# Kernel optimization log

Measured on AMD Instinct MI355X. Metric: run time of the kernel, lower is better.

Reference implementation:

```python
import jax, jax.numpy as jnp
from jax import lax
import numpy as np

NUM_ITER = 10
SMOOTH = 1.0
BCE_W, DICE_W, CLDICE_W = 0.3, 0.3, 0.4


def _maxpool(x, wh, ww):
    # x: (B, 1, H, W); 'SAME' padding with -inf identity == F.max_pool2d with zero-like pad of padding=(wh//2, ww//2)
    return lax.reduce_window(x, -jnp.inf, lax.max,
                             (1, 1, wh, ww), (1, 1, 1, 1), 'SAME')


def soft_erode(x):
    # min over vertical 3x1 and horizontal 1x3 windows, then elementwise min
    p1 = -_maxpool(-x, 3, 1)
    p2 = -_maxpool(-x, 1, 3)
    return jnp.minimum(p1, p2)


def soft_dilate(x):
    return _maxpool(x, 3, 3)


def soft_open(x):
    return soft_dilate(soft_erode(x))


def soft_skeleton(x):
    skel = jax.nn.relu(x - soft_open(x))
    er = x
    for _ in range(NUM_ITER):  # fixed, small trip count -> unrolled
        er = soft_erode(er)
        delta = jax.nn.relu(er - soft_open(er))
        skel = skel + jax.nn.relu(delta - skel * delta)
    return skel


def setup_inputs() -> dict:
    key = jax.random.key(0)
    k1, k2 = jax.random.split(key)
    B, H, W = 16, 1024, 1024
    pred = jax.random.normal(k1, (B, 1, H, W), dtype=jnp.float32)
    target = (jax.random.uniform(k2, (B, 1, H, W)) < 0.3).astype(jnp.float32)
    return {"pred": pred, "target": target}


def reference(pred, target):
    p = jax.nn.sigmoid(pred)
    y = target
    # BCEWithLogitsLoss (mean reduction, no pos_weight)
    bce = -jnp.mean(y * jax.nn.log_sigmoid(pred) + (1.0 - y) * jax.nn.log_sigmoid(-pred))
    # soft Dice over flattened tensors
    inter = jnp.sum(p * y)
    dice = (2.0 * inter + SMOOTH) / (jnp.sum(p) + jnp.sum(y) + SMOOTH)
    dice_loss = 1.0 - dice
    # clDice via soft skeletonization of both maps
    skel_pred = soft_skeleton(p)
    skel_tgt = soft_skeleton(y)
    tprec = (jnp.sum(skel_pred * y) + SMOOTH) / (jnp.sum(skel_pred) + SMOOTH)
    tsens = (jnp.sum(skel_tgt * p) + SMOOTH) / (jnp.sum(skel_tgt) + SMOOTH)
    cl_dice = 2.0 * tprec * tsens / (tprec + tsens + 1e-07)
    cldice_loss = 1.0 - cl_dice
    return BCE_W * bce + DICE_W * dice_loss + CLDICE_W * cldice_loss
```

## Files before the change

### kernel.cpp

```cpp
#include <hip/hip_runtime.h>
#include <hip/hip_fp16.h>
#include <math.h>

#define H_IMG 1024
#define W_IMG 1024
#define N_B   16
#define NPIX  (H_IMG * W_IMG)
#define N_TOT (16LL * NPIX)

#define TILE 64
#define HALO 12
#define RG   88
#define HST  92
#define SLOTS 32

#define PK_NINF 0xFC00FC00u
#define PK_SGN  0x80008000u

__device__ __forceinline__ float sigm(float x)  { return 1.0f / (1.0f + __expf(-x)); }

__device__ __forceinline__ unsigned pk_min(unsigned a, unsigned b) {
    unsigned r; asm("v_pk_min_f16 %0, %1, %2" : "=v"(r) : "v"(a), "v"(b)); return r;
}
__device__ __forceinline__ unsigned pk_max(unsigned a, unsigned b) {
    unsigned r; asm("v_pk_max_f16 %0, %1, %2" : "=v"(r) : "v"(a), "v"(b)); return r;
}
__device__ __forceinline__ unsigned pk_add(unsigned a, unsigned b) {
    unsigned r; asm("v_pk_add_f16 %0, %1, %2" : "=v"(r) : "v"(a), "v"(b)); return r;
}
__device__ __forceinline__ unsigned pk_fma(unsigned a, unsigned b, unsigned c) {
    unsigned r; asm("v_pk_fma_f16 %0, %1, %2, %3" : "=v"(r) : "v"(a), "v"(b), "v"(c)); return r;
}
__device__ __forceinline__ unsigned alignb(unsigned hi, unsigned lo) {
    unsigned r; asm("v_alignbit_b32 %0, %1, %2, 16" : "=v"(r) : "v"(hi), "v"(lo)); return r;
}

union H2U { __half2 h; unsigned u; };

__device__ __forceinline__ uint2 ld2u(const __half* p) { return *(const uint2*)p; }
__device__ __forceinline__ void  st2u(__half* p, unsigned a, unsigned b) { *(uint2*)p = make_uint2(a, b); }
__device__ __forceinline__ void st4h(__half* p, float x, float y, float z, float w) {
    H2U a, b;
    a.h = __floats2half2_rn(x, y);
    b.h = __floats2half2_rn(z, w);
    *(uint2*)p = make_uint2(a.u, b.u);
}

__device__ __forceinline__ void band_fix_inf(__half* b, int r0, int c0, int tid)
{
    unsigned short* u = (unsigned short*)b;
    const unsigned short val = 0x7C00;
    if (r0 == 0) {
        for (int idx = tid; idx < HALO * RG; idx += 512) {
            const int r = idx / RG, c = idx - r * RG;
            u[r * HST + c] = val;
        }
    }
    if (r0 == H_IMG - TILE) {
        for (int idx = tid; idx < HALO * RG; idx += 512) {
            const int r = idx / RG, c = idx - r * RG;
            u[(RG - HALO + r) * HST + c] = val;
        }
    }
    if (c0 == 0) {
        for (int idx = tid; idx < RG * HALO; idx += 512) {
            const int r = idx / HALO, c = idx - r * HALO;
            u[r * HST + c] = val;
        }
    }
    if (c0 == W_IMG - TILE) {
        for (int idx = tid; idx < RG * HALO; idx += 512) {
            const int r = idx / HALO, c = idx - r * HALO;
            u[r * HST + (RG - HALO + c)] = val;
        }
    }
}

template<bool SIG_SRC, bool SIG_OTH, bool DO_BCE, int CBASE>
__device__ __forceinline__
void skel_core(const float* __restrict__ src, const float* __restrict__ oth,
               double* __restrict__ acc, __half* cur, __half* nxt, float* red,
               int z, int r0, int c0, int tid, int bid)
{
    const float* s = src + (size_t)z * NPIX;

    {
        const int st = tid & 15, c = 4 * st;
        const int gc = c0 - HALO + c;
        const bool vec = (gc >= 0) && (gc + 3 < W_IMG);
        for (int r = tid >> 4; r < RG; r += 32) {
            const int gr = min(max(r0 - HALO + r, 0), H_IMG - 1);
            const float* row = s + (size_t)gr * W_IMG;
            float4 v;
            if (vec) v = *(const float4*)&row[gc];
            else {
                v.x = row[min(max(gc + 0, 0), W_IMG - 1)];
                v.y = row[min(max(gc + 1, 0), W_IMG - 1)];
                v.z = row[min(max(gc + 2, 0), W_IMG - 1)];
                v.w = row[min(max(gc + 3, 0), W_IMG - 1)];
            }
            if (SIG_SRC) { v.x = sigm(v.x); v.y = sigm(v.y); v.z = sigm(v.z); v.w = sigm(v.w); }
            st4h(&cur[r * HST + c], v.x, v.y, v.z, v.w);
        }
    }
    {
        const int st = 16 + (tid & 7);
        if (st < 23) {
            const int c = 4 * st, gc = c0 - HALO + c;
            const bool vec = (gc >= 0) && (gc + 3 < W_IMG);
            for (int r = tid >> 3; r < RG; r += 64) {
                const int gr = min(max(r0 - HALO + r, 0), H_IMG - 1);
                const float* row = s + (size_t)gr * W_IMG;
                float4 v;
                if (vec) v = *(const float4*)&row[gc];
                else {
                    v.x = row[min(max(gc + 0, 0), W_IMG - 1)];
                    v.y = row[min(max(gc + 1, 0), W_IMG - 1)];
                    v.z = row[min(max(gc + 2, 0), W_IMG - 1)];
                    v.w = row[min(max(gc + 3, 0), W_IMG - 1)];
                }
                if (SIG_SRC) { v.x = sigm(v.x); v.y = sigm(v.y); v.z = sigm(v.z); v.w = sigm(v.w); }
                st4h(&cur[r * HST + c], v.x, v.y, v.z, v.w);
            }
        }
    }
    __syncthreads();

    const bool edge = (r0 == 0) | (c0 == 0) | (r0 == H_IMG - TILE) | (c0 == W_IMG - TILE);

    unsigned skA01 = 0, skA23 = 0, skB01 = 0, skB23 = 0;

    const int oy = tid >> 3;
    const int j  = tid & 7;
    const int rr = HALO + oy;

    for (int k = 0; k < 11; ++k) {
        if (edge) { band_fix_inf(cur, r0, c0, tid); __syncthreads(); }

        const int rlo = k + 1, rhi = RG - 1 - k;
        const int sA = rlo >> 2, sE = (rhi + 3) >> 2;

        {
            const int l  = tid & 15;
            const int st = sA + l;
            const int c  = 4 * st;
            const int gcb = c0 - HALO + c;
            const bool cOOB = ((unsigned)gcb > (unsigned)(W_IMG - 4));
            for (int r = rlo + (tid >> 4); r < rhi; r += 32) {
                const int base = r * HST + c;
                const uint2 mid = ld2u(&cur[base]);
                const uint2 up  = ld2u(&cur[base - HST]);
                const uint2 dn  = ld2u(&cur[base + HST]);
                unsigned lfreg = (unsigned)__shfl_up((int)mid.y, 1);
                unsigned rtreg = (unsigned)__shfl_down((int)mid.x, 1);
                if (l == 0)  lfreg = ((unsigned)*(const unsigned short*)(cur + base - 1)) << 16;
                if (l == 15) rtreg = (unsigned)*(const unsigned short*)(cur + base + 4);
                const unsigned L01 = alignb(mid.x, lfreg);
                const unsigned L23 = alignb(mid.y, mid.x);
                const unsigned R23 = alignb(rtreg, mid.y);
                unsigned e01 = pk_min(pk_min(pk_min(up.x, dn.x), mid.x), pk_min(L01, L23));
                unsigned e23 = pk_min(pk_min(pk_min(up.y, dn.y), mid.y), pk_min(L23, R23));
                if (edge) {
                    const int gr = r0 - HALO + r;
                    if (((unsigned)gr >= (unsigned)H_IMG) | cOOB) { e01 = PK_NINF; e23 = PK_NINF; }
                }
                st2u(&nxt[base], e01, e23);
            }
        }
        {
            const int l  = tid & 7;
            const int st = sA + 16 + l;
            if (st < sE) {
                const int c = 4 * st;
                const int gcb = c0 - HALO + c;
                const bool cOOB  = ((unsigned)gcb > (unsigned)(W_IMG - 4));
                const bool lastS = (st == sE - 1);
                for (int r = rlo + (tid >> 3); r < rhi; r += 64) {
                    const int base = r * HST + c;
                    const uint2 mid = ld2u(&cur[base]);
                    const uint2 up  = ld2u(&cur[base - HST]);
                    const uint2 dn  = ld2u(&cur[base + HST]);
                    unsigned lfreg = (unsigned)__shfl_up((int)mid.y, 1);
                    unsigned rtreg = (unsigned)__shfl_down((int)mid.x, 1);
                    if (l == 0)  lfreg = ((unsigned)*(const unsigned short*)(cur + base - 1)) << 16;
                    if (lastS)   rtreg = (unsigned)*(const unsigned short*)(cur + base + 4);
                    const unsigned L01 = alignb(mid.x, lfreg);
                    const unsigned L23 = alignb(mid.y, mid.x);
                    const unsigned R23 = alignb(rtreg, mid.y);
                    unsigned e01 = pk_min(pk_min(pk_min(up.x, dn.x), mid.x), pk_min(L01, L23));
                    unsigned e23 = pk_min(pk_min(pk_min(up.y, dn.y), mid.y), pk_min(L23, R23));
                    if (edge) {
                        const int gr = r0 - HALO + r;
                        if (((unsigned)gr >= (unsigned)H_IMG) | cOOB) { e01 = PK_NINF; e23 = PK_NINF; }
                    }
                    st2u(&nxt[base], e01, e23);
                }
            }
        }
        __syncthreads();

        {
            const int cA = HALO + 4 * j;
            const int cB = cA + 32;
            const int bA = rr * HST + cA;
            const int bB = rr * HST + cB;
            const uint2 a0 = ld2u(&nxt[bA - HST]);
            const uint2 m0 = ld2u(&nxt[bA]);
            const uint2 d0 = ld2u(&nxt[bA + HST]);
            const uint2 a1 = ld2u(&nxt[bB - HST]);
            const uint2 m1 = ld2u(&nxt[bB]);
            const uint2 d1 = ld2u(&nxt[bB + HST]);
            const unsigned VA01 = pk_max(pk_max(a0.x, m0.x), d0.x);
            const unsigned VA23 = pk_max(pk_max(a0.y, m0.y), d0.y);
            const unsigned VB01 = pk_max(pk_max(a1.x, m1.x), d1.x);
            const unsigned VB23 = pk_max(pk_max(a1.y, m1.y), d1.y);
            unsigned vlA = (unsigned)__shfl_up((int)VA23, 1);
            const unsigned vrAa = (unsigned)__shfl_down((int)VA01, 1);
            const unsigned vrAb = (unsigned)__shfl_up((int)VB01, 7);
            unsigned vrA = (j == 7) ? vrAb : vrAa;
            const unsigned vlBa = (unsigned)__shfl_up((int)VB23, 1);
            const unsigned vlBb = (unsigned)__shfl_down((int)VA23, 7);
            unsigned vlB = (j == 0) ? vlBb : vlBa;
            unsigned vrB = (unsigned)__shfl_down((int)VB01, 1);
            if (j == 0) {
                const unsigned t1 = *(const unsigned short*)(nxt + bA - HST - 1);
                const unsigned t2 = *(const unsigned short*)(nxt + bA - 1);
                const unsigned t3 = *(const unsigned short*)(nxt + bA + HST - 1);
                vlA = pk_max(pk_max(t1, t2), t3) << 16;
            }
            if (j == 7) {
                const unsigned t1 = *(const unsigned short*)(nxt + bB - HST + 4);
                const unsigned t2 = *(const unsigned short*)(nxt + bB + 4);
                const unsigned t3 = *(const unsigned short*)(nxt + bB + HST + 4);
                vrB = pk_max(pk_max(t1, t2), t3);
            }
            const unsigned LA = alignb(VA01, vlA);
            const unsigned MA = alignb(VA23, VA01);
            const unsigned RA = alignb(vrA,  VA23);
            const unsigned oA01 = pk_max(pk_max(LA, MA), VA01);
            const unsigned oA23 = pk_max(pk_max(MA, RA), VA23);
            const unsigned LB = alignb(VB01, vlB);
            const unsigned MB = alignb(VB23, VB01);
            const unsigned RB = alignb(vrB,  VB23);
            const unsigned oB01 = pk_max(pk_max(LB, MB), VB01);
            const unsigned oB23 = pk_max(pk_max(MB, RB), VB23);
            const uint2 eA = ld2u(&cur[bA]);
            const uint2 eB = ld2u(&cur[bB]);
            unsigned d, u;
            d = pk_max(pk_add(eA.x, oA01 ^ PK_SGN), 0u);
            u = pk_max(pk_fma(skA01 ^ PK_SGN, d, d), 0u);
            skA01 = pk_add(skA01, u);
            d = pk_max(pk_add(eA.y, oA23 ^ PK_SGN), 0u);
            u = pk_max(pk_fma(skA23 ^ PK_SGN, d, d), 0u);
            skA23 = pk_add(skA23, u);
            d = pk_max(pk_add(eB.x, oB01 ^ PK_SGN), 0u);
            u = pk_max(pk_fma(skB01 ^ PK_SGN, d, d), 0u);
            skB01 = pk_add(skB01, u);
            d = pk_max(pk_add(eB.y, oB23 ^ PK_SGN), 0u);
            u = pk_max(pk_fma(skB23 ^ PK_SGN, d, d), 0u);
            skB23 = pk_add(skB23, u);
        }
        __syncthreads();

        __half* tp = cur; cur = nxt; nxt = tp;
    }

    float skf[8];
    {
        H2U u; float2 f;
        u.u = skA01; f = __half22float2(u.h); skf[0] = f.x; skf[1] = f.y;
        u.u = skA23; f = __half22float2(u.h); skf[2] = f.x; skf[3] = f.y;
        u.u = skB01; f = __half22float2(u.h); skf[4] = f.x; skf[5] = f.y;
        u.u = skB23; f = __half22float2(u.h); skf[6] = f.x; skf[7] = f.y;
    }

    const size_t gbase = (size_t)z * NPIX + (size_t)(r0 + oy) * W_IMG + c0;
    const float* op = oth + gbase;
    const float* pp = src + gbase;
    float ss = 0.f, sso = 0.f, sb = 0.f, sp = 0.f, sy = 0.f, spy = 0.f;
    #pragma unroll
    for (int t = 0; t < 2; ++t) {
        const int cc = 4 * (j + 8 * t);
        float4 ov = *(const float4*)&op[cc];
        float o0 = ov.x, o1 = ov.y, o2 = ov.z, o3 = ov.w;
        if (SIG_OTH) { o0 = sigm(o0); o1 = sigm(o1); o2 = sigm(o2); o3 = sigm(o3); }
        const float s0 = skf[4*t], s1 = skf[4*t+1], s2 = skf[4*t+2], s3 = skf[4*t+3];
        ss  += s0 + s1 + s2 + s3;
        sso += s0 * o0 + s1 * o1 + s2 * o2 + s3 * o3;
        if (DO_BCE) {
            const float4 xv = *(const float4*)&pp[cc];
            const float xs[4] = {xv.x, xv.y, xv.z, xv.w};
            const float ys[4] = {o0, o1, o2, o3};
            #pragma unroll
            for (int q = 0; q < 4; ++q) {
                const float x = xs[q], y = ys[q];
                const float zz = __expf(-fabsf(x));
                const float inv = 1.0f / (1.0f + zz);
                sb += fmaxf(x, 0.f) + __logf(1.0f + zz) - y * x;
                const float p = (x >= 0.f) ? inv : zz * inv;
                sp += p; sy += y; spy += p * y;
            }
        }
    }
    for (int off = 32; off > 0; off >>= 1) {
        ss  += __shfl_down(ss,  off);
        sso += __shfl_down(sso, off);
        if (DO_BCE) {
            sb  += __shfl_down(sb,  off);
            sp  += __shfl_down(sp,  off);
            sy  += __shfl_down(sy,  off);
            spy += __shfl_down(spy, off);
        }
    }
    const int wid = tid >> 6, lane = tid & 63;
    if (lane == 0) {
        red[0 * 8 + wid] = ss;  red[1 * 8 + wid] = sso;
        if (DO_BCE) {
            red[2 * 8 + wid] = sb;  red[3 * 8 + wid] = sp;
            red[4 * 8 + wid] = sy;  red[5 * 8 + wid] = spy;
        }
    }
    __syncthreads();
    if (tid == 0) {
        double SS = 0, SO = 0, B0 = 0, B1 = 0, B2 = 0, B3 = 0;
        for (int w = 0; w < 8; ++w) {
            SS += (double)red[0 * 8 + w];  SO += (double)red[1 * 8 + w];
            if (DO_BCE) {
                B0 += (double)red[2 * 8 + w]; B1 += (double)red[3 * 8 + w];
                B2 += (double)red[4 * 8 + w]; B3 += (double)red[5 * 8 + w];
            }
        }
        const int slot = bid & (SLOTS - 1);
        atomicAdd(&acc[slot * 8 + CBASE],     SS);
        atomicAdd(&acc[slot * 8 + CBASE + 1], SO);
        if (DO_BCE) {
            atomicAdd(&acc[slot * 8 + 0], B0);
            atomicAdd(&acc[slot * 8 + 1], B1);
            atomicAdd(&acc[slot * 8 + 2], B2);
            atomicAdd(&acc[slot * 8 + 3], B3);
        }
    }
}

__device__ __forceinline__
void bool_core(const float* __restrict__ tgt, const float* __restrict__ pred,
               double* __restrict__ acc, unsigned* bb, float* red,
               int z, int r0, int c0, int tid, int bid)
{
    unsigned* A  = bb;
    unsigned* B  = bb + RG * 4;
    unsigned* SK = bb + RG * 8;
    const float* tz = tgt + (size_t)z * NPIX;

    {
        const int wv = tid >> 6, ln = tid & 63;
        for (int r = wv; r < RG; r += 8) {
            const int gr = min(max(r0 - HALO + r, 0), H_IMG - 1);
            const float* row = tz + (size_t)gr * W_IMG;
            const int gc = c0 - HALO + ln;
            const float v = row[min(max(gc, 0), W_IMG - 1)];
            const unsigned long long b0 = __ballot(v > 0.5f);
            float v2 = 0.f;
            if (ln < 24) v2 = row[min(max(gc + 64, 0), W_IMG - 1)];
            const unsigned long long b1 = __ballot((ln < 24) && (v2 > 0.5f));
            if (ln < 4) {
                const unsigned val = (ln == 0) ? (unsigned)b0
                                   : (ln == 1) ? (unsigned)(b0 >> 32)
                                   : (ln == 2) ? (unsigned)b1 : 0u;
                A[r * 4 + ln] = val;
            }
        }
    }
    __syncthreads();

    const int r = tid >> 2, w = tid & 3;
    const bool act = (tid < RG * 4);

    const int gcb = c0 - HALO + 32 * w;
    unsigned cm = 0;
    {
        const int lo = -gcb;
        if (lo > 0) cm |= (lo >= 32) ? 0xFFFFFFFFu : ((1u << lo) - 1u);
        const int hs = W_IMG - gcb;
        if (hs < 32) cm |= (hs <= 0) ? 0xFFFFFFFFu : ~((1u << hs) - 1u);
    }
    const int grs = r0 - HALO + r;
    const unsigned Mself = cm | ((((unsigned)grs)       >= (unsigned)H_IMG) ? 0xFFFFFFFFu : 0u);
    const unsigned Mup   = cm | ((((unsigned)(grs - 1)) >= (unsigned)H_IMG) ? 0xFFFFFFFFu : 0u);
    const unsigned Mdn   = cm | ((((unsigned)(grs + 1)) >= (unsigned)H_IMG) ? 0xFFFFFFFFu : 0u);
    const unsigned KILL  = ~Mself;

    const int iu = max(r - 1, 0) * 4 + w;
    const int id = min(r + 1, RG - 1) * 4 + w;

    unsigned mid  = act ? A[r * 4 + w] : 0u;
    unsigned skel = 0u;
    unsigned* sB = A; unsigned* dB = B;

    for (int k = 0; k < 11; ++k) {
        const unsigned me = mid | Mself;
        unsigned up = 0xFFFFFFFFu, dn = 0xFFFFFFFFu;
        if (act) { up = sB[iu] | Mup; dn = sB[id] | Mdn; }
        const unsigned pv = (unsigned)__shfl_up((int)me, 1);
        const unsigned nx = (unsigned)__shfl_down((int)me, 1);
        const unsigned Lh = (me << 1) | (pv >> 31);
        const unsigned Rh = (me >> 1) | (nx << 31);
        const unsigned e  = (me & up & dn & Lh & Rh) & KILL;
        if (act) dB[r * 4 + w] = e;
        __syncthreads();
        unsigned eu = 0, ed = 0;
        if (act) { eu = dB[iu]; ed = dB[id]; }
        const unsigned V  = e | eu | ed;
        const unsigned pV = (unsigned)__shfl_up((int)V, 1);
        const unsigned nV = (unsigned)__shfl_down((int)V, 1);
        const unsigned open = V | ((V << 1) | (pV >> 31)) | ((V >> 1) | (nV << 31));
        skel |= mid & ~open;
        mid = e;
        unsigned* tp = sB; sB = dB; dB = tp;
    }
    if (act) SK[r * 4 + w] = skel;
    __syncthreads();

    const int oy = tid >> 3, j = tid & 7;
    const size_t gbase = (size_t)z * NPIX + (size_t)(r0 + oy) * W_IMG + c0;
    const float* pp = pred + gbase;
    float ss = 0.f, sso = 0.f;
    #pragma unroll
    for (int t = 0; t < 2; ++t) {
        const int cc  = 4 * (j + 8 * t);
        const int rcb = HALO + cc;
        const unsigned wd = SK[(HALO + oy) * 4 + (rcb >> 5)] >> (rcb & 31);
        const float4 xv = *(const float4*)&pp[cc];
        const float p0 = sigm(xv.x), p1 = sigm(xv.y), p2 = sigm(xv.z), p3 = sigm(xv.w);
        const float b0 = (float)( wd       & 1u);
        const float b1 = (float)((wd >> 1) & 1u);
        const float b2 = (float)((wd >> 2) & 1u);
        const float b3 = (float)((wd >> 3) & 1u);
        ss  += b0 + b1 + b2 + b3;
        sso += b0 * p0 + b1 * p1 + b2 * p2 + b3 * p3;
    }
    for (int off = 32; off > 0; off >>= 1) {
        ss  += __shfl_down(ss,  off);
        sso += __shfl_down(sso, off);
    }
    const int wid = tid >> 6, lane = tid & 63;
    if (lane == 0) { red[0 * 8 + wid] = ss; red[1 * 8 + wid] = sso; }
    __syncthreads();
    if (tid == 0) {
        double SS = 0, SO = 0;
        for (int wq = 0; wq < 8; ++wq) { SS += (double)red[0 * 8 + wq]; SO += (double)red[1 * 8 + wq]; }
        const int slot = bid & (SLOTS - 1);
        atomicAdd(&acc[slot * 8 + 6], SS);
        atomicAdd(&acc[slot * 8 + 7], SO);
    }
}

__global__ __launch_bounds__(512, 8)
void skel_all(const float* __restrict__ pred, const float* __restrict__ tgt,
              double* __restrict__ acc)
{
    __shared__ __align__(16) __half buf0[RG * HST];
    __shared__ __align__(16) __half buf1[RG * HST];
    __shared__ float red[48];
    const int tid = threadIdx.x;
    const int r0 = blockIdx.y * TILE, c0 = blockIdx.x * TILE;
    const int bid = ((int)blockIdx.z & 15) * 256 + blockIdx.y * 16 + blockIdx.x;
    if ((int)blockIdx.z < N_B)
        skel_core<true, false, true, 4>(pred, tgt, acc, buf0, buf1, red,
                                        blockIdx.z, r0, c0, tid, bid);
    else
        bool_core(tgt, pred, acc, (unsigned*)buf0, red,
                  (int)blockIdx.z - N_B, r0, c0, tid, bid);
}

__global__ void zero_acc(double* acc) { acc[threadIdx.x] = 0.0; }

__global__ void finalize_k(const double* __restrict__ acc, float* __restrict__ out)
{
    __shared__ double S[8];
    const int jj = threadIdx.x;
    if (jj < 8) {
        double t = 0.0;
        for (int s = 0; s < SLOTS; ++s) t += acc[s * 8 + jj];
        S[jj] = t;
    }
    __syncthreads();
    if (jj == 0) {
        const double bce   = S[0] / (double)N_TOT;
        const double dice  = (2.0 * S[3] + 1.0) / (S[1] + S[2] + 1.0);
        const double tprec = (S[5] + 1.0) / (S[4] + 1.0);
        const double tsens = (S[7] + 1.0) / (S[6] + 1.0);
        const double cl    = 2.0 * tprec * tsens / (tprec + tsens + 1e-7);
        out[0] = (float)(0.3 * bce + 0.3 * (1.0 - dice) + 0.4 * (1.0 - cl));
    }
}

extern "C" void kernel_launch(void* const* d_in, const int* in_sizes, int n_in,
                              void* d_out, int out_size, void* d_ws, size_t ws_size,
                              hipStream_t stream)
{
    const float* pred = (const float*)d_in[0];
    const float* tgt  = (const float*)d_in[1];
    float* out = (float*)d_out;
    double* acc = (double*)d_ws;

    zero_acc<<<1, SLOTS * 8, 0, stream>>>(acc);

    const dim3 grid(W_IMG / TILE, H_IMG / TILE, 2 * N_B);
    skel_all<<<grid, 512, 0, stream>>>(pred, tgt, acc);

    finalize_k<<<1, 64, 0, stream>>>(acc, out);
}
```

Before: 259.4 us.

## Pipeline erode and dilate to halve barriers on interior skeleton tiles

Interior tiles now run the erode of step k+1 in the same phase as the dilate/open of step k, using double buffers, so each iteration needs one barrier instead of two. Interior tiles also skip the border -inf fix-up and the out-of-bounds checks through a templated erode step. Edge tiles keep the original two-barrier ordering. This cuts synchronisation and the edge-handling overhead inside the eleven-step loop, at the cost of extra code size and more live registers for the carried erode values.

```diff
diff --git a/kernel.cpp b/kernel.cpp
--- a/kernel.cpp
+++ b/kernel.cpp
@@ -76,13 +76,140 @@
     }
 }
 
-template<bool SIG_SRC, bool SIG_OTH, bool DO_BCE, int CBASE>
+template<bool EDGE>
 __device__ __forceinline__
-void skel_core(const float* __restrict__ src, const float* __restrict__ oth,
-               double* __restrict__ acc, __half* cur, __half* nxt, float* red,
-               int z, int r0, int c0, int tid, int bid)
-{
-    const float* s = src + (size_t)z * NPIX;
+void erode_step(const __half* cur, __half* nxt, int k, int r0, int c0, int tid)
+{
+    const int rlo = k + 1, rhi = RG - 1 - k;
+    const int sA = rlo >> 2, sE = (rhi + 3) >> 2;
+
+    {
+        const int l  = tid & 15;
+        const int st = sA + l;
+        const int c  = 4 * st;
+        bool cOOB = false;
+        if (EDGE) {
+            const int gcb = c0 - HALO + c;
+            cOOB = ((unsigned)gcb > (unsigned)(W_IMG - 4));
+        }
+        for (int r = rlo + (tid >> 4); r < rhi; r += 32) {
+            const int base = r * HST + c;
+            const uint2 mid = ld2u(&cur[base]);
+            const uint2 up  = ld2u(&cur[base - HST]);
+            const uint2 dn  = ld2u(&cur[base + HST]);
+            unsigned lfreg = (unsigned)__shfl_up((int)mid.y, 1);
+            unsigned rtreg = (unsigned)__shfl_down((int)mid.x, 1);
+            if (l == 0)  lfreg = ((unsigned)*(const unsigned short*)(cur + base - 1)) << 16;
+            if (l == 15) rtreg = (unsigned)*(const unsigned short*)(cur + base + 4);
+            const unsigned L01 = alignb(mid.x, lfreg);
+            const unsigned L23 = alignb(mid.y, mid.x);
+            const unsigned R23 = alignb(rtreg, mid.y);
+            unsigned e01 = pk_min(pk_min(pk_min(up.x, dn.x), mid.x), pk_min(L01, L23));
+            unsigned e23 = pk_min(pk_min(pk_min(up.y, dn.y), mid.y), pk_min(L23, R23));
+            if (EDGE) {
+                const int gr = r0 - HALO + r;
+                if (((unsigned)gr >= (unsigned)H_IMG) | cOOB) { e01 = PK_NINF; e23 = PK_NINF; }
+            }
+            st2u(&nxt[base], e01, e23);
+        }
+    }
+    {
+        const int l  = tid & 7;
+        const int st = sA + 16 + l;
+        if (st < sE) {
+            const int c = 4 * st;
+            bool cOOB = false;
+            if (EDGE) {
+                const int gcb = c0 - HALO + c;
+                cOOB = ((unsigned)gcb > (unsigned)(W_IMG - 4));
+            }
+            const bool lastS = (st == sE - 1);
+            for (int r = rlo + (tid >> 3); r < rhi; r += 64) {
+                const int base = r * HST + c;
+                const uint2 mid = ld2u(&cur[base]);
+                const uint2 up  = ld2u(&cur[base - HST]);
+                const uint2 dn  = ld2u(&cur[base + HST]);
+                unsigned lfreg = (unsigned)__shfl_up((int)mid.y, 1);
+                unsigned rtreg = (unsigned)__shfl_down((int)mid.x, 1);
+                if (l == 0)  lfreg = ((unsigned)*(const unsigned short*)(cur + base - 1)) << 16;
+                if (lastS)   rtreg = (unsigned)*(const unsigned short*)(cur + base + 4);
+                const unsigned L01 = alignb(mid.x, lfreg);
+                const unsigned L23 = alignb(mid.y, mid.x);
+                const unsigned R23 = alignb(rtreg, mid.y);
+                unsigned e01 = pk_min(pk_min(pk_min(up.x, dn.x), mid.x), pk_min(L01, L23));
+                unsigned e23 = pk_min(pk_min(pk_min(up.y, dn.y), mid.y), pk_min(L23, R23));
+                if (EDGE) {
+                    const int gr = r0 - HALO + r;
+                    if (((unsigned)gr >= (unsigned)H_IMG) | cOOB) { e01 = PK_NINF; e23 = PK_NINF; }
+                }
+                st2u(&nxt[base], e01, e23);
+            }
+        }
+    }
+}
+
+struct OpenV { unsigned oA01, oA23, oB01, oB23; uint2 m0, m1; };
+
+__device__ __forceinline__
+OpenV dilate_open(const __half* buf, int bA, int bB, int j)
+{
+    OpenV R;
+    const uint2 a0 = ld2u(&buf[bA - HST]);
+    R.m0           = ld2u(&buf[bA]);
+    const uint2 d0 = ld2u(&buf[bA + HST]);
+    const uint2 a1 = ld2u(&buf[bB - HST]);
+    R.m1           = ld2u(&buf[bB]);
+    const uint2 d1 = ld2u(&buf[bB + HST]);
+    const unsigned VA01 = pk_max(pk_max(a0.x, R.m0.x), d0.x);
+    const unsigned VA23 = pk_max(pk_max(a0.y, R.m0.y), d0.y);
+    const unsigned VB01 = pk_max(pk_max(a1.x, R.m1.x), d1.x);
+    const unsigned VB23 = pk_max(pk_max(a1.y, R.m1.y), d1.y);
+    unsigned vlA = (unsigned)__shfl_up((int)VA23, 1);
+    const unsigned vrAa = (unsigned)__shfl_down((int)VA01, 1);
+    const unsigned vrAb = (unsigned)__shfl_up((int)VB01, 7);
+    unsigned vrA = (j == 7) ? vrAb : vrAa;
+    const unsigned vlBa = (unsigned)__shfl_up((int)VB23, 1);
+    const unsigned vlBb = (unsigned)__shfl_down((int)VA23, 7);
+    unsigned vlB = (j == 0) ? vlBb : vlBa;
+    unsigned vrB = (unsigned)__shfl_down((int)VB01, 1);
+    if (j == 0) {
+        const unsigned t1 = *(const unsigned short*)(buf + bA - HST - 1);
+        const unsigned t2 = *(const unsigned short*)(buf + bA - 1);
+        const unsigned t3 = *(const unsigned short*)(buf + bA + HST - 1);
+        vlA = pk_max(pk_max(t1, t2), t3) << 16;
+    }
+    if (j == 7) {
+        const unsigned t1 = *(const unsigned short*)(buf + bB - HST + 4);
+        const unsigned t2 = *(const unsigned short*)(buf + bB + 4);
+        const unsigned t3 = *(const unsigned short*)(buf + bB + HST + 4);
+        vrB = pk_max(pk_max(t1, t2), t3);
+    }
+    const unsigned LA = alignb(VA01, vlA);
+    const unsigned MA = alignb(VA23, VA01);
+    const unsigned RA = alignb(vrA,  VA23);
+    R.oA01 = pk_max(pk_max(LA, MA), VA01);
+    R.oA23 = pk_max(pk_max(MA, RA), VA23);
+    const unsigned LB = alignb(VB01, vlB);
+    const unsigned MB = alignb(VB23, VB01);
+    const unsigned RB = alignb(vrB,  VB23);
+    R.oB01 = pk_max(pk_max(LB, MB), VB01);
+    R.oB23 = pk_max(pk_max(MB, RB), VB23);
+    return R;
+}
+
+__device__ __forceinline__ void skel_upd(unsigned& sk, unsigned e, unsigned o)
+{
+    const unsigned d = pk_max(pk_add(e, o ^ PK_SGN), 0u);
+    const unsigned u = pk_max(pk_fma(sk ^ PK_SGN, d, d), 0u);
+    sk = pk_add(sk, u);
+}
+
+__device__ __forceinline__
+void skel_f16(const float* __restrict__ pred, const float* __restrict__ tgt,
+              double* __restrict__ acc, __half* cur, __half* nxt, float* red,
+              int z, int r0, int c0, int tid, int bid)
+{
+    const float* s = pred + (size_t)z * NPIX;
 
     {
         const int st = tid & 15, c = 4 * st;
@@ -99,8 +226,7 @@
                 v.z = row[min(max(gc + 2, 0), W_IMG - 1)];
                 v.w = row[min(max(gc + 3, 0), W_IMG - 1)];
             }
-            if (SIG_SRC) { v.x = sigm(v.x); v.y = sigm(v.y); v.z = sigm(v.z); v.w = sigm(v.w); }
-            st4h(&cur[r * HST + c], v.x, v.y, v.z, v.w);
+            st4h(&cur[r * HST + c], sigm(v.x), sigm(v.y), sigm(v.z), sigm(v.w));
         }
     }
     {
@@ -119,8 +245,7 @@
                     v.z = row[min(max(gc + 2, 0), W_IMG - 1)];
                     v.w = row[min(max(gc + 3, 0), W_IMG - 1)];
                 }
-                if (SIG_SRC) { v.x = sigm(v.x); v.y = sigm(v.y); v.z = sigm(v.z); v.w = sigm(v.w); }
-                st4h(&cur[r * HST + c], v.x, v.y, v.z, v.w);
+                st4h(&cur[r * HST + c], sigm(v.x), sigm(v.y), sigm(v.z), sigm(v.w));
             }
         }
     }
@@ -133,136 +258,49 @@
     const int oy = tid >> 3;
     const int j  = tid & 7;
     const int rr = HALO + oy;
-
-    for (int k = 0; k < 11; ++k) {
-        if (edge) { band_fix_inf(cur, r0, c0, tid); __syncthreads(); }
-
-        const int rlo = k + 1, rhi = RG - 1 - k;
-        const int sA = rlo >> 2, sE = (rhi + 3) >> 2;
-
-        {
-            const int l  = tid & 15;
-            const int st = sA + l;
-            const int c  = 4 * st;
-            const int gcb = c0 - HALO + c;
-            const bool cOOB = ((unsigned)gcb > (unsigned)(W_IMG - 4));
-            for (int r = rlo + (tid >> 4); r < rhi; r += 32) {
-                const int base = r * HST + c;
-                const uint2 mid = ld2u(&cur[base]);
-                const uint2 up  = ld2u(&cur[base - HST]);
-                const uint2 dn  = ld2u(&cur[base + HST]);
-                unsigned lfreg = (unsigned)__shfl_up((int)mid.y, 1);
-                unsigned rtreg = (unsigned)__shfl_down((int)mid.x, 1);
-                if (l == 0)  lfreg = ((unsigned)*(const unsigned short*)(cur + base - 1)) << 16;
-                if (l == 15) rtreg = (unsigned)*(const unsigned short*)(cur + base + 4);
-                const unsigned L01 = alignb(mid.x, lfreg);
-                const unsigned L23 = alignb(mid.y, mid.x);
-                const unsigned R23 = alignb(rtreg, mid.y);
-                unsigned e01 = pk_min(pk_min(pk_min(up.x, dn.x), mid.x), pk_min(L01, L23));
-                unsigned e23 = pk_min(pk_min(pk_min(up.y, dn.y), mid.y), pk_min(L23, R23));
-                if (edge) {
-                    const int gr = r0 - HALO + r;
-                    if (((unsigned)gr >= (unsigned)H_IMG) | cOOB) { e01 = PK_NINF; e23 = PK_NINF; }
-                }
-                st2u(&nxt[base], e01, e23);
-            }
-        }
-        {
-            const int l  = tid & 7;
-            const int st = sA + 16 + l;
-            if (st < sE) {
-                const int c = 4 * st;
-                const int gcb = c0 - HALO + c;
-                const bool cOOB  = ((unsigned)gcb > (unsigned)(W_IMG - 4));
-                const bool lastS = (st == sE - 1);
-                for (int r = rlo + (tid >> 3); r < rhi; r += 64) {
-                    const int base = r * HST + c;
-                    const uint2 mid = ld2u(&cur[base]);
-                    const uint2 up  = ld2u(&cur[base - HST]);
-                    const uint2 dn  = ld2u(&cur[base + HST]);
-                    unsigned lfreg = (unsigned)__shfl_up((int)mid.y, 1);
-                    unsigned rtreg = (unsigned)__shfl_down((int)mid.x, 1);
-                    if (l == 0)  lfreg = ((unsigned)*(const unsigned short*)(cur + base - 1)) << 16;
-                    if (lastS)   rtreg = (unsigned)*(const unsigned short*)(cur + base + 4);
-                    const unsigned L01 = alignb(mid.x, lfreg);
-                    const unsigned L23 = alignb(mid.y, mid.x);
-                    const unsigned R23 = alignb(rtreg, mid.y);
-                    unsigned e01 = pk_min(pk_min(pk_min(up.x, dn.x), mid.x), pk_min(L01, L23));
-                    unsigned e23 = pk_min(pk_min(pk_min(up.y, dn.y), mid.y), pk_min(L23, R23));
-                    if (edge) {
-                        const int gr = r0 - HALO + r;
-                        if (((unsigned)gr >= (unsigned)H_IMG) | cOOB) { e01 = PK_NINF; e23 = PK_NINF; }
-                    }
-                    st2u(&nxt[base], e01, e23);
-                }
-            }
-        }
+    const int bA = rr * HST + HALO + 4 * j;
+    const int bB = bA + 32;
+
+    if (!edge) {
+        uint2 eA, eB;
+        erode_step<false>(cur, nxt, 0, r0, c0, tid);
+        eA = ld2u(&cur[bA]); eB = ld2u(&cur[bB]);
         __syncthreads();
-
-        {
-            const int cA = HALO + 4 * j;
-            const int cB = cA + 32;
-            const int bA = rr * HST + cA;
-            const int bB = rr * HST + cB;
-            const uint2 a0 = ld2u(&nxt[bA - HST]);
-            const uint2 m0 = ld2u(&nxt[bA]);
-            const uint2 d0 = ld2u(&nxt[bA + HST]);
-            const uint2 a1 = ld2u(&nxt[bB - HST]);
-            const uint2 m1 = ld2u(&nxt[bB]);
-            const uint2 d1 = ld2u(&nxt[bB + HST]);
-            const unsigned VA01 = pk_max(pk_max(a0.x, m0.x), d0.x);
-            const unsigned VA23 = pk_max(pk_max(a0.y, m0.y), d0.y);
-            const unsigned VB01 = pk_max(pk_max(a1.x, m1.x), d1.x);
-            const unsigned VB23 = pk_max(pk_max(a1.y, m1.y), d1.y);
-            unsigned vlA = (unsigned)__shfl_up((int)VA23, 1);
-            const unsigned vrAa = (unsigned)__shfl_down((int)VA01, 1);
-            const unsigned vrAb = (unsigned)__shfl_up((int)VB01, 7);
-            unsigned vrA = (j == 7) ? vrAb : vrAa;
-            const unsigned vlBa = (unsigned)__shfl_up((int)VB23, 1);
-            const unsigned vlBb = (unsigned)__shfl_down((int)VA23, 7);
-            unsigned vlB = (j == 0) ? vlBb : vlBa;
-            unsigned vrB = (unsigned)__shfl_down((int)VB01, 1);
-            if (j == 0) {
-                const unsigned t1 = *(const unsigned short*)(nxt + bA - HST - 1);
-                const unsigned t2 = *(const unsigned short*)(nxt + bA - 1);
-                const unsigned t3 = *(const unsigned short*)(nxt + bA + HST - 1);
-                vlA = pk_max(pk_max(t1, t2), t3) << 16;
-            }
-            if (j == 7) {
-                const unsigned t1 = *(const unsigned short*)(nxt + bB - HST + 4);
-                const unsigned t2 = *(const unsigned short*)(nxt + bB + 4);
-                const unsigned t3 = *(const unsigned short*)(nxt + bB + HST + 4);
-                vrB = pk_max(pk_max(t1, t2), t3);
-            }
-            const unsigned LA = alignb(VA01, vlA);
-            const unsigned MA = alignb(VA23, VA01);
-            const unsigned RA = alignb(vrA,  VA23);
-            const unsigned oA01 = pk_max(pk_max(LA, MA), VA01);
-            const unsigned oA23 = pk_max(pk_max(MA, RA), VA23);
-            const unsigned LB = alignb(VB01, vlB);
-            const unsigned MB = alignb(VB23, VB01);
-            const unsigned RB = alignb(vrB,  VB23);
-            const unsigned oB01 = pk_max(pk_max(LB, MB), VB01);
-            const unsigned oB23 = pk_max(pk_max(MB, RB), VB23);
+        { __half* tp = cur; cur = nxt; nxt = tp; }
+        #pragma unroll 1
+        for (int sps = 1; sps <= 10; ++sps) {
+            const OpenV R = dilate_open(cur, bA, bB, j);
+            skel_upd(skA01, eA.x, R.oA01);
+            skel_upd(skA23, eA.y, R.oA23);
+            skel_upd(skB01, eB.x, R.oB01);
+            skel_upd(skB23, eB.y, R.oB23);
+            eA = R.m0; eB = R.m1;
+            erode_step<false>(cur, nxt, sps, r0, c0, tid);
+            __syncthreads();
+            { __half* tp = cur; cur = nxt; nxt = tp; }
+        }
+        const OpenV R = dilate_open(cur, bA, bB, j);
+        skel_upd(skA01, eA.x, R.oA01);
+        skel_upd(skA23, eA.y, R.oA23);
+        skel_upd(skB01, eB.x, R.oB01);
+        skel_upd(skB23, eB.y, R.oB23);
+    } else {
+        #pragma unroll 1
+        for (int k = 0; k <= 10; ++k) {
+            band_fix_inf(cur, r0, c0, tid);
+            __syncthreads();
+            erode_step<true>(cur, nxt, k, r0, c0, tid);
+            __syncthreads();
+            const OpenV R = dilate_open(nxt, bA, bB, j);
             const uint2 eA = ld2u(&cur[bA]);
             const uint2 eB = ld2u(&cur[bB]);
-            unsigned d, u;
-            d = pk_max(pk_add(eA.x, oA01 ^ PK_SGN), 0u);
-            u = pk_max(pk_fma(skA01 ^ PK_SGN, d, d), 0u);
-            skA01 = pk_add(skA01, u);
-            d = pk_max(pk_add(eA.y, oA23 ^ PK_SGN), 0u);
-            u = pk_max(pk_fma(skA23 ^ PK_SGN, d, d), 0u);
-            skA23 = pk_add(skA23, u);
-            d = pk_max(pk_add(eB.x, oB01 ^ PK_SGN), 0u);
-            u = pk_max(pk_fma(skB01 ^ PK_SGN, d, d), 0u);
-            skB01 = pk_add(skB01, u);
-            d = pk_max(pk_add(eB.y, oB23 ^ PK_SGN), 0u);
-            u = pk_max(pk_fma(skB23 ^ PK_SGN, d, d), 0u);
-            skB23 = pk_add(skB23, u);
-        }
-        __syncthreads();
-
-        __half* tp = cur; cur = nxt; nxt = tp;
+            skel_upd(skA01, eA.x, R.oA01);
+            skel_upd(skA23, eA.y, R.oA23);
+            skel_upd(skB01, eB.x, R.oB01);
+            skel_upd(skB23, eB.y, R.oB23);
+            __syncthreads();
+            __half* tp = cur; cur = nxt; nxt = tp;
+        }
     }
 
     float skf[8];
@@ -275,70 +313,59 @@
     }
 
     const size_t gbase = (size_t)z * NPIX + (size_t)(r0 + oy) * W_IMG + c0;
-    const float* op = oth + gbase;
-    const float* pp = src + gbase;
+    const float* op = tgt  + gbase;
+    const float* pp = pred + gbase;
     float ss = 0.f, sso = 0.f, sb = 0.f, sp = 0.f, sy = 0.f, spy = 0.f;
     #pragma unroll
     for (int t = 0; t < 2; ++t) {
         const int cc = 4 * (j + 8 * t);
-        float4 ov = *(const float4*)&op[cc];
-        float o0 = ov.x, o1 = ov.y, o2 = ov.z, o3 = ov.w;
-        if (SIG_OTH) { o0 = sigm(o0); o1 = sigm(o1); o2 = sigm(o2); o3 = sigm(o3); }
+        const float4 ov = *(const float4*)&op[cc];
+        const float o0 = ov.x, o1 = ov.y, o2 = ov.z, o3 = ov.w;
         const float s0 = skf[4*t], s1 = skf[4*t+1], s2 = skf[4*t+2], s3 = skf[4*t+3];
         ss  += s0 + s1 + s2 + s3;
         sso += s0 * o0 + s1 * o1 + s2 * o2 + s3 * o3;
-        if (DO_BCE) {
-            const float4 xv = *(const float4*)&pp[cc];
-            const float xs[4] = {xv.x, xv.y, xv.z, xv.w};
-            const float ys[4] = {o0, o1, o2, o3};
-            #pragma unroll
-            for (int q = 0; q < 4; ++q) {
-                const float x = xs[q], y = ys[q];
-                const float zz = __expf(-fabsf(x));
-                const float inv = 1.0f / (1.0f + zz);
-                sb += fmaxf(x, 0.f) + __logf(1.0f + zz) - y * x;
-                const float p = (x >= 0.f) ? inv : zz * inv;
-                sp += p; sy += y; spy += p * y;
-            }
+        const float4 xv = *(const float4*)&pp[cc];
+        const float xs[4] = {xv.x, xv.y, xv.z, xv.w};
+        const float ys[4] = {o0, o1, o2, o3};
+        #pragma unroll
+        for (int q = 0; q < 4; ++q) {
+            const float x = xs[q], y = ys[q];
+            const float zz = __expf(-fabsf(x));
+            const float inv = 1.0f / (1.0f + zz);
+            sb += fmaxf(x, 0.f) + __logf(1.0f + zz) - y * x;
+            const float p = (x >= 0.f) ? inv : zz * inv;
+            sp += p; sy += y; spy += p * y;
         }
     }
     for (int off = 32; off > 0; off >>= 1) {
         ss  += __shfl_down(ss,  off);
         sso += __shfl_down(sso, off);
-        if (DO_BCE) {
-            sb  += __shfl_down(sb,  off);
-            sp  += __shfl_down(sp,  off);
-            sy  += __shfl_down(sy,  off);
-            spy += __shfl_down(spy, off);
-        }
+        sb  += __shfl_down(sb,  off);
+        sp  += __shfl_down(sp,  off);
+        sy  += __shfl_down(sy,  off);
+        spy += __shfl_down(spy, off);
     }
     const int wid = tid >> 6, lane = tid & 63;
     if (lane == 0) {
         red[0 * 8 + wid] = ss;  red[1 * 8 + wid] = sso;
-        if (DO_BCE) {
-            red[2 * 8 + wid] = sb;  red[3 * 8 + wid] = sp;
-            red[4 * 8 + wid] = sy;  red[5 * 8 + wid] = spy;
-        }
+        red[2 * 8 + wid] = sb;  red[3 * 8 + wid] = sp;
+        red[4 * 8 + wid] = sy;  red[5 * 8 + wid] = spy;
     }
     __syncthreads();
     if (tid == 0) {
         double SS = 0, SO = 0, B0 = 0, B1 = 0, B2 = 0, B3 = 0;
         for (int w = 0; w < 8; ++w) {
             SS += (double)red[0 * 8 + w];  SO += (double)red[1 * 8 + w];
-            if (DO_BCE) {
-                B0 += (double)red[2 * 8 + w]; B1 += (double)red[3 * 8 + w];
-                B2 += (double)red[4 * 8 + w]; B3 += (double)red[5 * 8 + w];
-            }
+            B0 += (double)red[2 * 8 + w];  B1 += (double)red[3 * 8 + w];
+            B2 += (double)red[4 * 8 + w];  B3 += (double)red[5 * 8 + w];
         }
         const int slot = bid & (SLOTS - 1);
-        atomicAdd(&acc[slot * 8 + CBASE],     SS);
-        atomicAdd(&acc[slot * 8 + CBASE + 1], SO);
-        if (DO_BCE) {
-            atomicAdd(&acc[slot * 8 + 0], B0);
-            atomicAdd(&acc[slot * 8 + 1], B1);
-            atomicAdd(&acc[slot * 8 + 2], B2);
-            atomicAdd(&acc[slot * 8 + 3], B3);
-        }
+        atomicAdd(&acc[slot * 8 + 4], SS);
+        atomicAdd(&acc[slot * 8 + 5], SO);
+        atomicAdd(&acc[slot * 8 + 0], B0);
+        atomicAdd(&acc[slot * 8 + 1], B1);
+        atomicAdd(&acc[slot * 8 + 2], B2);
+        atomicAdd(&acc[slot * 8 + 3], B3);
     }
 }
 
@@ -466,8 +493,7 @@
     const int r0 = blockIdx.y * TILE, c0 = blockIdx.x * TILE;
     const int bid = ((int)blockIdx.z & 15) * 256 + blockIdx.y * 16 + blockIdx.x;
     if ((int)blockIdx.z < N_B)
-        skel_core<true, false, true, 4>(pred, tgt, acc, buf0, buf1, red,
-                                        blockIdx.z, r0, c0, tid, bid);
+        skel_f16(pred, tgt, acc, buf0, buf1, red, blockIdx.z, r0, c0, tid, bid);
     else
         bool_core(tgt, pred, acc, (unsigned*)buf0, red,
                   (int)blockIdx.z - N_B, r0, c0, tid, bid);
```

Result: slower. 268.2 us (+3.4%).
